# Kernel optimization log

Hardware: AMD Instinct MI355X
Metric: run time of the kernel (lower is better)

Reference implementation:

```python
import jax, jax.numpy as jnp
import numpy as np

T, N, F, S = 512, 64, 256, 1024  # seq_len, batch, behavior features, lstm size


def setup_inputs() -> dict:
    key = jax.random.key(0)
    k1, k2, k3 = jax.random.split(key, 3)
    x = jax.random.normal(k1, (T, N, F), dtype=jnp.float32)
    # stacked gate weights: order [i, f, g, o]
    Wx = jax.random.normal(k2, (4, F, S), dtype=jnp.float32) * 0.02
    Wh = jax.random.normal(k3, (4, S, S), dtype=jnp.float32) * 0.02
    b = jnp.zeros((4, S), dtype=jnp.float32)
    return {"x": x, "Wx": Wx, "Wh": Wh, "b": b}


def reference(x, Wx, Wh, b):
    # x: [T, n, f]; Wx: [4, f, s]; Wh: [4, s, s]; b: [4, s]
    n = x.shape[1]
    s = Wh.shape[-1]
    h0 = jnp.zeros((n, s), dtype=x.dtype)
    c0 = jnp.zeros((n, s), dtype=x.dtype)

    def step(carry, xt):
        h, c = carry
        # fused 4-gate projection: z[k] = xt @ Wx[k] + h @ Wh[k] + b[k]
        z = (jnp.einsum('nf,kfs->kns', xt, Wx)
             + jnp.einsum('ns,kst->knt', h, Wh)
             + b[:, None, :])  # [4, n, s]
        i = jax.nn.sigmoid(z[0])
        f = jax.nn.sigmoid(z[1])
        g = jnp.tanh(z[2])
        o = jax.nn.sigmoid(z[3])
        c = f * c + i * g
        h = o * jnp.tanh(c)
        return (h, c), h

    (_, _), hs = jax.lax.scan(step, (h0, c0), x)
    return hs  # [T, n, s]
```

## Files before the change

### kernel.cpp

```cpp
#include <hip/hip_runtime.h>
#include <hip/hip_bf16.h>

#define T_LEN 512
#define NB 64
#define FB 256
#define SB 1024
#define NWG 256

typedef __attribute__((ext_vector_type(8))) short bf16x8;
typedef __attribute__((ext_vector_type(4))) float f32x4;

#define MFMA(a, b, c) __builtin_amdgcn_mfma_f32_16x16x32_bf16((a), (b), (c), 0, 0, 0)

__device__ __forceinline__ float fast_sigmoid(float z) {
    return 1.f / (1.f + __expf(-z));
}
__device__ __forceinline__ float fast_tanh(float z) {
    return 1.f - 2.f / (1.f + __expf(2.f * z));
}

__device__ __forceinline__ bf16x8 load_frag_dev(const __hip_bfloat16* p) {
    const unsigned long long* q = (const unsigned long long*)p;
    unsigned long long a = __hip_atomic_load(q,     __ATOMIC_RELAXED, __HIP_MEMORY_SCOPE_AGENT);
    unsigned long long b = __hip_atomic_load(q + 1, __ATOMIC_RELAXED, __HIP_MEMORY_SCOPE_AGENT);
    union { unsigned long long u[2]; bf16x8 v; } r;
    r.u[0] = a; r.u[1] = b;
    return r.v;
}

__global__ void xfrag_kernel(const float* __restrict__ x, __hip_bfloat16* __restrict__ xaf) {
    int tid  = blockIdx.x * 256 + threadIdx.x;
    int l    = tid & 63;
    int frag = tid >> 6;
    int kc   = frag & 7;
    int m    = (frag >> 3) & 3;
    int t    = frag >> 5;
    int row  = m * 16 + (l & 15);
    int k0   = kc * 32 + 8 * (l >> 4);
    const float* src = x + ((size_t)(t * NB + row)) * FB + k0;
    __hip_bfloat16* dst = xaf + (size_t)frag * 512 + l * 8;
#pragma unroll
    for (int e = 0; e < 8; ++e) dst[e] = __float2bfloat16(src[e]);
}

__global__ void wfrag_kernel(const float* __restrict__ Wx, const float* __restrict__ Wh,
                             __hip_bfloat16* __restrict__ wbf) {
    int tid  = blockIdx.x * 256 + threadIdx.x;
    int l    = tid & 63;
    int frag = tid >> 6;
    int g    = frag & 3;
    int kcw  = (frag >> 2) % 10;
    int wv   = (frag / 40) & 3;
    int sb   = frag / 160;
    int kc   = (kcw < 2) ? (wv * 2 + kcw) : (8 + wv * 8 + (kcw - 2));
    int s    = sb * 16 + (l & 15);
    int k0   = kc * 32 + 8 * (l >> 4);
    __hip_bfloat16* dst = wbf + (size_t)frag * 512 + l * 8;
#pragma unroll
    for (int e = 0; e < 8; ++e) {
        int k = k0 + e;
        float v = (k < FB) ? Wx[((size_t)g * FB + k) * SB + s]
                           : Wh[((size_t)g * SB + (k - FB)) * SB + s];
        dst[e] = __float2bfloat16(v);
    }
}

__global__ __launch_bounds__(256, 1) void lstm_persist(
    const __hip_bfloat16* __restrict__ xaf,
    const __hip_bfloat16* __restrict__ wbf,
    const float* __restrict__ bias,
    __hip_bfloat16* __restrict__ hfrag,
    float* __restrict__ cbuf,
    float* __restrict__ out,
    unsigned int* __restrict__ flag,
    int t0, int nsteps, int use_sync)
{
    __shared__ float part[4 * 16 * 4 * 17];
    const int tid = threadIdx.x;
    const int wv  = tid >> 6;
    const int l   = tid & 63;
    const int ng  = blockIdx.x >> 6;
    const int sb  = blockIdx.x & 63;
    const int lr  = l & 15;
    const int lg  = l >> 4;

    const int fidx = (ng * 64 + wv * 16 + (l & 15)) * 2;

    const int gn = tid >> 4;
    const int sc = tid & 15;

    bf16x8 wf[40];
    {
        const __hip_bfloat16* wp = wbf + ((size_t)(sb * 4 + wv) * 40) * 512 + l * 8;
#pragma unroll
        for (int i = 0; i < 40; ++i) wf[i] = *reinterpret_cast<const bf16x8*>(wp + (size_t)i * 512);
    }
    float br[4];
#pragma unroll
    for (int g = 0; g < 4; ++g) br[g] = bias[g * SB + sb * 16 + sc];
    float creg = cbuf[(ng * 16 + gn) * SB + sb * 16 + sc];

    const int k8   = 16 * (sb & 1) + sc;
    const int lane = (k8 >> 3) * 16 + gn;
    const size_t hoff = (size_t)((sb >> 1) * 4 + ng) * 512 + lane * 8 + (k8 & 7);

    f32x4 acc[4];
#pragma unroll
    for (int g = 0; g < 4; ++g) acc[g] = (f32x4){0.f, 0.f, 0.f, 0.f};
    {
        const __hip_bfloat16* xs = xaf + (size_t)t0 * 16384;
#pragma unroll
        for (int j = 0; j < 2; ++j) {
            int kc = wv * 2 + j;
            bf16x8 a = *reinterpret_cast<const bf16x8*>(xs + (size_t)(ng * 8 + kc) * 512 + l * 8);
#pragma unroll
            for (int g = 0; g < 4; ++g) acc[g] = MFMA(a, wf[j * 4 + g], acc[g]);
        }
    }

    for (int tt = 0; tt < nsteps; ++tt) {
        const int t = t0 + tt;

        if (use_sync && tt > 0) {
            const unsigned int* f1 = flag + (size_t)(t - 1) * 512;
            for (;;) {
                unsigned a = __hip_atomic_load(&f1[fidx], __ATOMIC_RELAXED, __HIP_MEMORY_SCOPE_AGENT);
                if (__all(a != 0)) break;
            }
            asm volatile("" ::: "memory");
        }

        const __hip_bfloat16* hs = hfrag + (size_t)(t & 3) * 65536;
#pragma unroll
        for (int j = 0; j < 8; ++j) {
            int kch = wv * 8 + j;
            bf16x8 a = load_frag_dev(hs + (size_t)(kch * 4 + ng) * 512 + l * 8);
#pragma unroll
            for (int g = 0; g < 4; ++g) acc[g] = MFMA(a, wf[(2 + j) * 4 + g], acc[g]);
        }

#pragma unroll
        for (int g = 0; g < 4; ++g)
#pragma unroll
            for (int i = 0; i < 4; ++i)
                part[((wv * 16 + lg * 4 + i) * 4 + g) * 17 + lr] = acc[g][i];
        __syncthreads();

        float hv;
        {
            float z[4];
#pragma unroll
            for (int g = 0; g < 4; ++g) {
                float s = 0.f;
#pragma unroll
                for (int w2 = 0; w2 < 4; ++w2)
                    s += part[((w2 * 16 + gn) * 4 + g) * 17 + sc];
                z[g] = s + br[g];
            }
            float ig = fast_sigmoid(z[0]);
            float fg = fast_sigmoid(z[1]);
            float gg = fast_tanh(z[2]);
            float og = fast_sigmoid(z[3]);
            float c  = fg * creg + ig * gg;
            hv       = og * fast_tanh(c);
            creg     = c;
            unsigned short hu = __bfloat16_as_ushort(__float2bfloat16(hv));
            unsigned short* hd = reinterpret_cast<unsigned short*>(
                hfrag + (size_t)((t + 1) & 3) * 65536) + hoff;
            __hip_atomic_store(hd, hu, __ATOMIC_RELAXED, __HIP_MEMORY_SCOPE_AGENT);
        }

        if (use_sync) {
            __syncthreads();
            if (tid == 0)
                __hip_atomic_store(&flag[((size_t)t * 256 + blockIdx.x) * 2], 1u,
                                   __ATOMIC_RELAXED, __HIP_MEMORY_SCOPE_AGENT);
        }

        out[(size_t)t * (NB * SB) + (size_t)(ng * 16 + gn) * SB + sb * 16 + sc] = hv;

        if (tt + 1 < nsteps) {
#pragma unroll
            for (int g = 0; g < 4; ++g) acc[g] = (f32x4){0.f, 0.f, 0.f, 0.f};
            const __hip_bfloat16* xs = xaf + (size_t)(t + 1) * 16384;
#pragma unroll
            for (int j = 0; j < 2; ++j) {
                int kc = wv * 2 + j;
                bf16x8 a = *reinterpret_cast<const bf16x8*>(xs + (size_t)(ng * 8 + kc) * 512 + l * 8);
#pragma unroll
                for (int g = 0; g < 4; ++g) acc[g] = MFMA(a, wf[j * 4 + g], acc[g]);
            }
        }
    }

    cbuf[(ng * 16 + gn) * SB + sb * 16 + sc] = creg;
}

extern "C" void kernel_launch(void* const* d_in, const int* in_sizes, int n_in,
                              void* d_out, int out_size, void* d_ws, size_t ws_size,
                              hipStream_t stream) {
    const float* x  = (const float*)d_in[0];
    const float* Wx = (const float*)d_in[1];
    const float* Wh = (const float*)d_in[2];
    const float* b  = (const float*)d_in[3];
    float* out = (float*)d_out;

    char* ws = (char*)d_ws;
    __hip_bfloat16* xaf   = (__hip_bfloat16*)ws;
    __hip_bfloat16* wbf   = (__hip_bfloat16*)(ws + 16777216);
    __hip_bfloat16* hfrag = (__hip_bfloat16*)(ws + 27262976);
    float*          cbuf  = (float*)(ws + 27787264);
    unsigned int*   flag  = (unsigned int*)(ws + 28049408);

    hipLaunchKernelGGL(xfrag_kernel, dim3(4096), dim3(256), 0, stream, x, xaf);
    hipLaunchKernelGGL(wfrag_kernel, dim3(2560), dim3(256), 0, stream, Wx, Wh, wbf);
    hipMemsetAsync(hfrag, 0, 524288, stream);
    hipMemsetAsync(cbuf, 0, 262144, stream);
    hipMemsetAsync(flag, 0, 1048576, stream);

    const __hip_bfloat16* p_xaf = xaf;
    const __hip_bfloat16* p_wbf = wbf;
    const float* p_bias = b;
    __hip_bfloat16* p_hfrag = hfrag;
    float* p_cbuf = cbuf;
    float* p_out = out;
    unsigned int* p_flag = flag;
    int z0 = 0, ns = T_LEN, us = 1;
    void* args[] = {&p_xaf, &p_wbf, &p_bias, &p_hfrag, &p_cbuf, &p_out, &p_flag, &z0, &ns, &us};
    hipError_t err = hipLaunchCooperativeKernel((void*)lstm_persist, dim3(NWG), dim3(256),
                                                args, 0, stream);
    if (err != hipSuccess) {
        for (int t = 0; t < T_LEN; ++t) {
            hipLaunchKernelGGL(lstm_persist, dim3(NWG), dim3(256), 0, stream,
                               xaf, wbf, b, hfrag, cbuf, out, flag, t, 1, 0);
        }
    }
}
```

Measured before the change: 1.267 ms.

## Halve persistent workgroups and pipeline two independent batch groups per block

Each workgroup now handles two batch groups (A and B) with the same register-resident weights, cutting the grid from 256 to 128 workgroups. The h buffer layout changes so each batch group has its own contiguous ring, and flags are tracked per batch group. Because A and B are independent recurrences, the wait for B's dependencies can overlap with A's gate computation and vice versa. The aim is to hide inter-workgroup synchronisation latency and to halve weight traffic per group. The cost is more serial work per workgroup and twice the accumulator registers.

```diff
diff --git a/kernel.cpp b/kernel.cpp
--- a/kernel.cpp
+++ b/kernel.cpp
@@ -5,7 +5,7 @@
 #define NB 64
 #define FB 256
 #define SB 1024
-#define NWG 256
+#define NWG 128
 
 typedef __attribute__((ext_vector_type(8))) short bf16x8;
 typedef __attribute__((ext_vector_type(4))) float f32x4;
@@ -79,12 +79,13 @@
     const int tid = threadIdx.x;
     const int wv  = tid >> 6;
     const int l   = tid & 63;
-    const int ng  = blockIdx.x >> 6;
+    const int p   = blockIdx.x >> 6;
     const int sb  = blockIdx.x & 63;
     const int lr  = l & 15;
     const int lg  = l >> 4;
-
-    const int fidx = (ng * 64 + wv * 16 + (l & 15)) * 2;
+    const int ngA = 2 * p, ngB = 2 * p + 1;
+
+    const int fbase = (p * 64 + wv * 16 + (l & 15)) * 4;
 
     const int gn = tid >> 4;
     const int sc = tid & 15;
@@ -98,102 +99,157 @@
     float br[4];
 #pragma unroll
     for (int g = 0; g < 4; ++g) br[g] = bias[g * SB + sb * 16 + sc];
-    float creg = cbuf[(ng * 16 + gn) * SB + sb * 16 + sc];
+    float cregA = cbuf[(ngA * 16 + gn) * SB + sb * 16 + sc];
+    float cregB = cbuf[(ngB * 16 + gn) * SB + sb * 16 + sc];
 
     const int k8   = 16 * (sb & 1) + sc;
     const int lane = (k8 >> 3) * 16 + gn;
-    const size_t hoff = (size_t)((sb >> 1) * 4 + ng) * 512 + lane * 8 + (k8 & 7);
-
-    f32x4 acc[4];
-#pragma unroll
-    for (int g = 0; g < 4; ++g) acc[g] = (f32x4){0.f, 0.f, 0.f, 0.f};
+    const int hoff = (sb >> 1) * 512 + lane * 8 + (k8 & 7);
+
+    f32x4 accA[4], accB[4];
+#pragma unroll
+    for (int g = 0; g < 4; ++g) { accA[g] = (f32x4){0,0,0,0}; accB[g] = (f32x4){0,0,0,0}; }
     {
         const __hip_bfloat16* xs = xaf + (size_t)t0 * 16384;
 #pragma unroll
         for (int j = 0; j < 2; ++j) {
             int kc = wv * 2 + j;
-            bf16x8 a = *reinterpret_cast<const bf16x8*>(xs + (size_t)(ng * 8 + kc) * 512 + l * 8);
-#pragma unroll
-            for (int g = 0; g < 4; ++g) acc[g] = MFMA(a, wf[j * 4 + g], acc[g]);
+            bf16x8 aA = *reinterpret_cast<const bf16x8*>(xs + (size_t)(ngA * 8 + kc) * 512 + l * 8);
+            bf16x8 aB = *reinterpret_cast<const bf16x8*>(xs + (size_t)(ngB * 8 + kc) * 512 + l * 8);
+#pragma unroll
+            for (int g = 0; g < 4; ++g) {
+                accA[g] = MFMA(aA, wf[j * 4 + g], accA[g]);
+                accB[g] = MFMA(aB, wf[j * 4 + g], accB[g]);
+            }
         }
     }
 
     for (int tt = 0; tt < nsteps; ++tt) {
         const int t = t0 + tt;
+        const __hip_bfloat16* hsA = hfrag + (size_t)ngA * 65536 + (size_t)(t & 3) * 16384;
+        const __hip_bfloat16* hsB = hfrag + (size_t)ngB * 65536 + (size_t)(t & 3) * 16384;
 
         if (use_sync && tt > 0) {
             const unsigned int* f1 = flag + (size_t)(t - 1) * 512;
             for (;;) {
-                unsigned a = __hip_atomic_load(&f1[fidx], __ATOMIC_RELAXED, __HIP_MEMORY_SCOPE_AGENT);
+                unsigned a = __hip_atomic_load(&f1[fbase], __ATOMIC_RELAXED, __HIP_MEMORY_SCOPE_AGENT);
                 if (__all(a != 0)) break;
             }
             asm volatile("" ::: "memory");
         }
-
-        const __hip_bfloat16* hs = hfrag + (size_t)(t & 3) * 65536;
 #pragma unroll
         for (int j = 0; j < 8; ++j) {
-            int kch = wv * 8 + j;
-            bf16x8 a = load_frag_dev(hs + (size_t)(kch * 4 + ng) * 512 + l * 8);
-#pragma unroll
-            for (int g = 0; g < 4; ++g) acc[g] = MFMA(a, wf[(2 + j) * 4 + g], acc[g]);
-        }
-
+            bf16x8 a = load_frag_dev(hsA + (size_t)(wv * 8 + j) * 512 + l * 8);
+#pragma unroll
+            for (int g = 0; g < 4; ++g) accA[g] = MFMA(a, wf[(2 + j) * 4 + g], accA[g]);
+        }
 #pragma unroll
         for (int g = 0; g < 4; ++g)
 #pragma unroll
             for (int i = 0; i < 4; ++i)
-                part[((wv * 16 + lg * 4 + i) * 4 + g) * 17 + lr] = acc[g][i];
+                part[((wv * 16 + lg * 4 + i) * 4 + g) * 17 + lr] = accA[g][i];
         __syncthreads();
-
-        float hv;
+        float hvA;
         {
             float z[4];
 #pragma unroll
             for (int g = 0; g < 4; ++g) {
                 float s = 0.f;
 #pragma unroll
-                for (int w2 = 0; w2 < 4; ++w2)
-                    s += part[((w2 * 16 + gn) * 4 + g) * 17 + sc];
+                for (int w2 = 0; w2 < 4; ++w2) s += part[((w2 * 16 + gn) * 4 + g) * 17 + sc];
                 z[g] = s + br[g];
             }
             float ig = fast_sigmoid(z[0]);
             float fg = fast_sigmoid(z[1]);
             float gg = fast_tanh(z[2]);
             float og = fast_sigmoid(z[3]);
-            float c  = fg * creg + ig * gg;
-            hv       = og * fast_tanh(c);
-            creg     = c;
-            unsigned short hu = __bfloat16_as_ushort(__float2bfloat16(hv));
+            float c  = fg * cregA + ig * gg;
+            hvA      = og * fast_tanh(c);
+            cregA    = c;
+            unsigned short hu = __bfloat16_as_ushort(__float2bfloat16(hvA));
             unsigned short* hd = reinterpret_cast<unsigned short*>(
-                hfrag + (size_t)((t + 1) & 3) * 65536) + hoff;
+                hfrag + (size_t)ngA * 65536 + (size_t)((t + 1) & 3) * 16384) + hoff;
             __hip_atomic_store(hd, hu, __ATOMIC_RELAXED, __HIP_MEMORY_SCOPE_AGENT);
         }
-
         if (use_sync) {
             __syncthreads();
             if (tid == 0)
-                __hip_atomic_store(&flag[((size_t)t * 256 + blockIdx.x) * 2], 1u,
+                __hip_atomic_store(&flag[((size_t)t * 128 + blockIdx.x) * 4], 1u,
                                    __ATOMIC_RELAXED, __HIP_MEMORY_SCOPE_AGENT);
         }
-
-        out[(size_t)t * (NB * SB) + (size_t)(ng * 16 + gn) * SB + sb * 16 + sc] = hv;
+        out[(size_t)t * (NB * SB) + (size_t)(ngA * 16 + gn) * SB + sb * 16 + sc] = hvA;
+
+        if (use_sync && tt > 0) {
+            const unsigned int* f1 = flag + (size_t)(t - 1) * 512;
+            for (;;) {
+                unsigned a = __hip_atomic_load(&f1[fbase + 1], __ATOMIC_RELAXED, __HIP_MEMORY_SCOPE_AGENT);
+                if (__all(a != 0)) break;
+            }
+            asm volatile("" ::: "memory");
+        }
+#pragma unroll
+        for (int j = 0; j < 8; ++j) {
+            bf16x8 a = load_frag_dev(hsB + (size_t)(wv * 8 + j) * 512 + l * 8);
+#pragma unroll
+            for (int g = 0; g < 4; ++g) accB[g] = MFMA(a, wf[(2 + j) * 4 + g], accB[g]);
+        }
+        if (!use_sync) __syncthreads();
+#pragma unroll
+        for (int g = 0; g < 4; ++g)
+#pragma unroll
+            for (int i = 0; i < 4; ++i)
+                part[((wv * 16 + lg * 4 + i) * 4 + g) * 17 + lr] = accB[g][i];
+        __syncthreads();
+        float hvB;
+        {
+            float z[4];
+#pragma unroll
+            for (int g = 0; g < 4; ++g) {
+                float s = 0.f;
+#pragma unroll
+                for (int w2 = 0; w2 < 4; ++w2) s += part[((w2 * 16 + gn) * 4 + g) * 17 + sc];
+                z[g] = s + br[g];
+            }
+            float ig = fast_sigmoid(z[0]);
+            float fg = fast_sigmoid(z[1]);
+            float gg = fast_tanh(z[2]);
+            float og = fast_sigmoid(z[3]);
+            float c  = fg * cregB + ig * gg;
+            hvB      = og * fast_tanh(c);
+            cregB    = c;
+            unsigned short hu = __bfloat16_as_ushort(__float2bfloat16(hvB));
+            unsigned short* hd = reinterpret_cast<unsigned short*>(
+                hfrag + (size_t)ngB * 65536 + (size_t)((t + 1) & 3) * 16384) + hoff;
+            __hip_atomic_store(hd, hu, __ATOMIC_RELAXED, __HIP_MEMORY_SCOPE_AGENT);
+        }
+        if (use_sync) {
+            __syncthreads();
+            if (tid == 0)
+                __hip_atomic_store(&flag[((size_t)t * 128 + blockIdx.x) * 4 + 1], 1u,
+                                   __ATOMIC_RELAXED, __HIP_MEMORY_SCOPE_AGENT);
+        }
+        out[(size_t)t * (NB * SB) + (size_t)(ngB * 16 + gn) * SB + sb * 16 + sc] = hvB;
 
         if (tt + 1 < nsteps) {
 #pragma unroll
-            for (int g = 0; g < 4; ++g) acc[g] = (f32x4){0.f, 0.f, 0.f, 0.f};
+            for (int g = 0; g < 4; ++g) { accA[g] = (f32x4){0,0,0,0}; accB[g] = (f32x4){0,0,0,0}; }
             const __hip_bfloat16* xs = xaf + (size_t)(t + 1) * 16384;
 #pragma unroll
             for (int j = 0; j < 2; ++j) {
                 int kc = wv * 2 + j;
-                bf16x8 a = *reinterpret_cast<const bf16x8*>(xs + (size_t)(ng * 8 + kc) * 512 + l * 8);
-#pragma unroll
-                for (int g = 0; g < 4; ++g) acc[g] = MFMA(a, wf[j * 4 + g], acc[g]);
-            }
-        }
-    }
-
-    cbuf[(ng * 16 + gn) * SB + sb * 16 + sc] = creg;
+                bf16x8 aA = *reinterpret_cast<const bf16x8*>(xs + (size_t)(ngA * 8 + kc) * 512 + l * 8);
+                bf16x8 aB = *reinterpret_cast<const bf16x8*>(xs + (size_t)(ngB * 8 + kc) * 512 + l * 8);
+#pragma unroll
+                for (int g = 0; g < 4; ++g) {
+                    accA[g] = MFMA(aA, wf[j * 4 + g], accA[g]);
+                    accB[g] = MFMA(aB, wf[j * 4 + g], accB[g]);
+                }
+            }
+        }
+    }
+
+    cbuf[(ngA * 16 + gn) * SB + sb * 16 + sc] = cregA;
+    cbuf[(ngB * 16 + gn) * SB + sb * 16 + sc] = cregB;
 }
 
 extern "C" void kernel_launch(void* const* d_in, const int* in_sizes, int n_in,
```

After: 3.397 ms. 168% more time.

## Replace per-step flag barrier with NaN-sentinel data-driven synchronization

Applied to the files above, without the earlier changes.

The new path gives every timestep its own h buffer, pre-filled with a bf16 NaN sentinel. Consumers spin directly on the h fragments until no sentinel remains, then feed the loaded values straight into MFMA. This removes the flag store, the extra __syncthreads, and the separate flag poll from each step's critical path. In exchange it needs a 64MB workspace plus a large sentinel-init kernel, and it would misbehave if a real h value were the sentinel NaN pattern. The old flag kernel stays as a fallback when the workspace is too small.

```diff
diff --git a/kernel.cpp b/kernel.cpp
--- a/kernel.cpp
+++ b/kernel.cpp
@@ -65,7 +65,147 @@
     }
 }
 
-__global__ __launch_bounds__(256, 1) void lstm_persist(
+__global__ void sentinit_kernel(uint4* __restrict__ p) {
+    p[blockIdx.x * 256 + threadIdx.x] =
+        (uint4){0x7FC07FC0u, 0x7FC07FC0u, 0x7FC07FC0u, 0x7FC07FC0u};
+}
+
+__global__ __launch_bounds__(256, 1) void lstm_ds(
+    const __hip_bfloat16* __restrict__ xaf,
+    const __hip_bfloat16* __restrict__ wbf,
+    const float* __restrict__ bias,
+    __hip_bfloat16* __restrict__ hfrag,
+    float* __restrict__ cbuf,
+    float* __restrict__ out,
+    int t0, int nsteps)
+{
+    __shared__ float part[2][4 * 16 * 4 * 17];
+    const int tid = threadIdx.x;
+    const int wv  = tid >> 6;
+    const int l   = tid & 63;
+    const int ng  = blockIdx.x >> 6;
+    const int sb  = blockIdx.x & 63;
+    const int lr  = l & 15;
+    const int lg  = l >> 4;
+
+    const int gn = tid >> 4;
+    const int sc = tid & 15;
+
+    bf16x8 wf[40];
+    {
+        const __hip_bfloat16* wp = wbf + ((size_t)(sb * 4 + wv) * 40) * 512 + l * 8;
+#pragma unroll
+        for (int i = 0; i < 40; ++i) wf[i] = *reinterpret_cast<const bf16x8*>(wp + (size_t)i * 512);
+    }
+    float br[4];
+#pragma unroll
+    for (int g = 0; g < 4; ++g) br[g] = bias[g * SB + sb * 16 + sc];
+    float creg = cbuf[(ng * 16 + gn) * SB + sb * 16 + sc];
+
+    const int k8   = 16 * (sb & 1) + sc;
+    const int lane = (k8 >> 3) * 16 + gn;
+    const size_t hoff = (size_t)((sb >> 1) * 4 + ng) * 512 + lane * 8 + (k8 & 7);
+
+    f32x4 acc[4];
+#pragma unroll
+    for (int g = 0; g < 4; ++g) acc[g] = (f32x4){0.f, 0.f, 0.f, 0.f};
+    {
+        const __hip_bfloat16* xs = xaf + (size_t)t0 * 16384;
+#pragma unroll
+        for (int j = 0; j < 2; ++j) {
+            int kc = wv * 2 + j;
+            bf16x8 a = *reinterpret_cast<const bf16x8*>(xs + (size_t)(ng * 8 + kc) * 512 + l * 8);
+#pragma unroll
+            for (int g = 0; g < 4; ++g) acc[g] = MFMA(a, wf[j * 4 + g], acc[g]);
+        }
+    }
+
+    for (int tt = 0; tt < nsteps; ++tt) {
+        const int t  = t0 + tt;
+        const int pb = t & 1;
+
+        const __hip_bfloat16* hs = hfrag + (size_t)t * 65536;
+        unsigned long long v[16];
+        for (;;) {
+#pragma unroll
+            for (int j = 0; j < 8; ++j) {
+                const unsigned long long* q = reinterpret_cast<const unsigned long long*>(
+                    hs + (size_t)((wv * 8 + j) * 4 + ng) * 512 + l * 8);
+                v[2 * j]     = __hip_atomic_load(q,     __ATOMIC_RELAXED, __HIP_MEMORY_SCOPE_AGENT);
+                v[2 * j + 1] = __hip_atomic_load(q + 1, __ATOMIC_RELAXED, __HIP_MEMORY_SCOPE_AGENT);
+            }
+            bool ok = true;
+#pragma unroll
+            for (int k = 0; k < 16; ++k) {
+                unsigned lo = (unsigned)v[k], hi = (unsigned)(v[k] >> 32);
+                ok = ok && ((lo & 0xFFFFu) != 0x7FC0u) && ((lo >> 16) != 0x7FC0u)
+                        && ((hi & 0xFFFFu) != 0x7FC0u) && ((hi >> 16) != 0x7FC0u);
+            }
+            if (__all(ok)) break;
+        }
+
+#pragma unroll
+        for (int j = 0; j < 8; ++j) {
+            union { unsigned long long u[2]; bf16x8 a; } ua;
+            ua.u[0] = v[2 * j];
+            ua.u[1] = v[2 * j + 1];
+#pragma unroll
+            for (int g = 0; g < 4; ++g) acc[g] = MFMA(ua.a, wf[(2 + j) * 4 + g], acc[g]);
+        }
+
+#pragma unroll
+        for (int g = 0; g < 4; ++g)
+#pragma unroll
+            for (int i = 0; i < 4; ++i)
+                part[pb][((wv * 16 + lg * 4 + i) * 4 + g) * 17 + lr] = acc[g][i];
+        __syncthreads();
+
+        float hv;
+        {
+            float z[4];
+#pragma unroll
+            for (int g = 0; g < 4; ++g) {
+                float s = 0.f;
+#pragma unroll
+                for (int w2 = 0; w2 < 4; ++w2)
+                    s += part[pb][((w2 * 16 + gn) * 4 + g) * 17 + sc];
+                z[g] = s + br[g];
+            }
+            float ig = fast_sigmoid(z[0]);
+            float fg = fast_sigmoid(z[1]);
+            float gg = fast_tanh(z[2]);
+            float og = fast_sigmoid(z[3]);
+            float c  = fg * creg + ig * gg;
+            hv       = og * fast_tanh(c);
+            creg     = c;
+            if (t + 1 < T_LEN) {
+                unsigned short hu = __bfloat16_as_ushort(__float2bfloat16(hv));
+                unsigned short* hd = reinterpret_cast<unsigned short*>(
+                    hfrag + (size_t)(t + 1) * 65536) + hoff;
+                __hip_atomic_store(hd, hu, __ATOMIC_RELAXED, __HIP_MEMORY_SCOPE_AGENT);
+            }
+        }
+
+        out[(size_t)t * (NB * SB) + (size_t)(ng * 16 + gn) * SB + sb * 16 + sc] = hv;
+
+        if (tt + 1 < nsteps) {
+#pragma unroll
+            for (int g = 0; g < 4; ++g) acc[g] = (f32x4){0.f, 0.f, 0.f, 0.f};
+            const __hip_bfloat16* xs = xaf + (size_t)(t + 1) * 16384;
+#pragma unroll
+            for (int j = 0; j < 2; ++j) {
+                int kc = wv * 2 + j;
+                bf16x8 a = *reinterpret_cast<const bf16x8*>(xs + (size_t)(ng * 8 + kc) * 512 + l * 8);
+#pragma unroll
+                for (int g = 0; g < 4; ++g) acc[g] = MFMA(a, wf[j * 4 + g], acc[g]);
+            }
+        }
+    }
+
+    cbuf[(ng * 16 + gn) * SB + sb * 16 + sc] = creg;
+}
+
+__global__ __launch_bounds__(256, 1) void lstm_fl(
     const __hip_bfloat16* __restrict__ xaf,
     const __hip_bfloat16* __restrict__ wbf,
     const float* __restrict__ bias,
@@ -83,9 +223,7 @@
     const int sb  = blockIdx.x & 63;
     const int lr  = l & 15;
     const int lg  = l >> 4;
-
     const int fidx = (ng * 64 + wv * 16 + (l & 15)) * 2;
-
     const int gn = tid >> 4;
     const int sc = tid & 15;
 
@@ -99,7 +237,6 @@
 #pragma unroll
     for (int g = 0; g < 4; ++g) br[g] = bias[g * SB + sb * 16 + sc];
     float creg = cbuf[(ng * 16 + gn) * SB + sb * 16 + sc];
-
     const int k8   = 16 * (sb & 1) + sc;
     const int lane = (k8 >> 3) * 16 + gn;
     const size_t hoff = (size_t)((sb >> 1) * 4 + ng) * 512 + lane * 8 + (k8 & 7);
@@ -120,7 +257,6 @@
 
     for (int tt = 0; tt < nsteps; ++tt) {
         const int t = t0 + tt;
-
         if (use_sync && tt > 0) {
             const unsigned int* f1 = flag + (size_t)(t - 1) * 512;
             for (;;) {
@@ -129,7 +265,6 @@
             }
             asm volatile("" ::: "memory");
         }
-
         const __hip_bfloat16* hs = hfrag + (size_t)(t & 3) * 65536;
 #pragma unroll
         for (int j = 0; j < 8; ++j) {
@@ -138,14 +273,12 @@
 #pragma unroll
             for (int g = 0; g < 4; ++g) acc[g] = MFMA(a, wf[(2 + j) * 4 + g], acc[g]);
         }
-
 #pragma unroll
         for (int g = 0; g < 4; ++g)
 #pragma unroll
             for (int i = 0; i < 4; ++i)
                 part[((wv * 16 + lg * 4 + i) * 4 + g) * 17 + lr] = acc[g][i];
         __syncthreads();
-
         float hv;
         {
             float z[4];
@@ -153,8 +286,7 @@
             for (int g = 0; g < 4; ++g) {
                 float s = 0.f;
 #pragma unroll
-                for (int w2 = 0; w2 < 4; ++w2)
-                    s += part[((w2 * 16 + gn) * 4 + g) * 17 + sc];
+                for (int w2 = 0; w2 < 4; ++w2) s += part[((w2 * 16 + gn) * 4 + g) * 17 + sc];
                 z[g] = s + br[g];
             }
             float ig = fast_sigmoid(z[0]);
@@ -169,16 +301,13 @@
                 hfrag + (size_t)((t + 1) & 3) * 65536) + hoff;
             __hip_atomic_store(hd, hu, __ATOMIC_RELAXED, __HIP_MEMORY_SCOPE_AGENT);
         }
-
         if (use_sync) {
             __syncthreads();
             if (tid == 0)
                 __hip_atomic_store(&flag[((size_t)t * 256 + blockIdx.x) * 2], 1u,
                                    __ATOMIC_RELAXED, __HIP_MEMORY_SCOPE_AGENT);
         }
-
         out[(size_t)t * (NB * SB) + (size_t)(ng * 16 + gn) * SB + sb * 16 + sc] = hv;
-
         if (tt + 1 < nsteps) {
 #pragma unroll
             for (int g = 0; g < 4; ++g) acc[g] = (f32x4){0.f, 0.f, 0.f, 0.f};
@@ -192,7 +321,6 @@
             }
         }
     }
-
     cbuf[(ng * 16 + gn) * SB + sb * 16 + sc] = creg;
 }
 
@@ -206,33 +334,64 @@
     float* out = (float*)d_out;
 
     char* ws = (char*)d_ws;
-    __hip_bfloat16* xaf   = (__hip_bfloat16*)ws;
-    __hip_bfloat16* wbf   = (__hip_bfloat16*)(ws + 16777216);
-    __hip_bfloat16* hfrag = (__hip_bfloat16*)(ws + 27262976);
-    float*          cbuf  = (float*)(ws + 27787264);
-    unsigned int*   flag  = (unsigned int*)(ws + 28049408);
+    __hip_bfloat16* xaf = (__hip_bfloat16*)ws;
+    __hip_bfloat16* wbf = (__hip_bfloat16*)(ws + 16777216);
 
     hipLaunchKernelGGL(xfrag_kernel, dim3(4096), dim3(256), 0, stream, x, xaf);
     hipLaunchKernelGGL(wfrag_kernel, dim3(2560), dim3(256), 0, stream, Wx, Wh, wbf);
-    hipMemsetAsync(hfrag, 0, 524288, stream);
-    hipMemsetAsync(cbuf, 0, 262144, stream);
-    hipMemsetAsync(flag, 0, 1048576, stream);
-
-    const __hip_bfloat16* p_xaf = xaf;
-    const __hip_bfloat16* p_wbf = wbf;
-    const float* p_bias = b;
-    __hip_bfloat16* p_hfrag = hfrag;
-    float* p_cbuf = cbuf;
-    float* p_out = out;
-    unsigned int* p_flag = flag;
-    int z0 = 0, ns = T_LEN, us = 1;
-    void* args[] = {&p_xaf, &p_wbf, &p_bias, &p_hfrag, &p_cbuf, &p_out, &p_flag, &z0, &ns, &us};
-    hipError_t err = hipLaunchCooperativeKernel((void*)lstm_persist, dim3(NWG), dim3(256),
-                                                args, 0, stream);
-    if (err != hipSuccess) {
-        for (int t = 0; t < T_LEN; ++t) {
-            hipLaunchKernelGGL(lstm_persist, dim3(NWG), dim3(256), 0, stream,
-                               xaf, wbf, b, hfrag, cbuf, out, flag, t, 1, 0);
-        }
-    }
-}
+
+    const size_t NEED = 16777216ULL + 10485760ULL + 67108864ULL + 262144ULL;
+
+    if (ws_size >= NEED) {
+        __hip_bfloat16* hfrag = (__hip_bfloat16*)(ws + 27262976);
+        float*          cbuf  = (float*)(ws + 94371840);
+
+        hipLaunchKernelGGL(sentinit_kernel, dim3(16352), dim3(256), 0, stream,
+                           (uint4*)(hfrag + 65536));
+        hipMemsetAsync(hfrag, 0, 131072, stream);
+        hipMemsetAsync(cbuf, 0, 262144, stream);
+
+        const __hip_bfloat16* p_xaf = xaf;
+        const __hip_bfloat16* p_wbf = wbf;
+        const float* p_bias = b;
+        __hip_bfloat16* p_hfrag = hfrag;
+        float* p_cbuf = cbuf;
+        float* p_out = out;
+        int z0 = 0, ns = T_LEN;
+        void* args[] = {&p_xaf, &p_wbf, &p_bias, &p_hfrag, &p_cbuf, &p_out, &z0, &ns};
+        hipError_t err = hipLaunchCooperativeKernel((void*)lstm_ds, dim3(NWG), dim3(256),
+                                                    args, 0, stream);
+        if (err != hipSuccess) {
+            for (int t = 0; t < T_LEN; ++t) {
+                hipLaunchKernelGGL(lstm_ds, dim3(NWG), dim3(256), 0, stream,
+                                   xaf, wbf, b, hfrag, cbuf, out, t, 1);
+            }
+        }
+    } else {
+        __hip_bfloat16* hfrag = (__hip_bfloat16*)(ws + 27262976);
+        float*          cbuf  = (float*)(ws + 27787264);
+        unsigned int*   flag  = (unsigned int*)(ws + 28049408);
+
+        hipMemsetAsync(hfrag, 0, 524288, stream);
+        hipMemsetAsync(cbuf, 0, 262144, stream);
+        hipMemsetAsync(flag, 0, 1048576, stream);
+
+        const __hip_bfloat16* p_xaf = xaf;
+        const __hip_bfloat16* p_wbf = wbf;
+        const float* p_bias = b;
+        __hip_bfloat16* p_hfrag = hfrag;
+        float* p_cbuf = cbuf;
+        float* p_out = out;
+        unsigned int* p_flag = flag;
+        int z0 = 0, ns = T_LEN, us = 1;
+        void* args[] = {&p_xaf, &p_wbf, &p_bias, &p_hfrag, &p_cbuf, &p_out, &p_flag, &z0, &ns, &us};
+        hipError_t err = hipLaunchCooperativeKernel((void*)lstm_fl, dim3(NWG), dim3(256),
+                                                    args, 0, stream);
+        if (err != hipSuccess) {
+            for (int t = 0; t < T_LEN; ++t) {
+                hipLaunchKernelGGL(lstm_fl, dim3(NWG), dim3(256), 0, stream,
+                                   xaf, wbf, b, hfrag, cbuf, out, flag, t, 1, 0);
+            }
+        }
+    }
+}
```

Measured after the change: 1.418 ms. +12.0%, slower.

## Poll NaN-sentinel hidden-state slots and drop the per-step block barrier

Applied to the files above, without the earlier changes.

The hidden-state buffer becomes one slot per timestep instead of a 4-deep ring, and every slot except the first is pre-filled with a bf16 NaN sentinel by a new init kernel. Each block now re-reads its h fragments until none of them hold the sentinel. Because the data itself is checked, the second __syncthreads before the flag store can go, and the LDS partial-sum buffer is double-buffered so the next step's writes cannot race the current reads. The per-block flag spin stays, so the sentinel check adds polling on top of it. The change also costs a 64MB sentinel fill per launch and assumes a real h value never equals the NaN pattern.

```diff
diff --git a/kernel.cpp b/kernel.cpp
--- a/kernel.cpp
+++ b/kernel.cpp
@@ -65,7 +65,12 @@
     }
 }
 
-__global__ __launch_bounds__(256, 1) void lstm_persist(
+__global__ void sentinit_kernel(uint4* __restrict__ p) {
+    p[blockIdx.x * 256 + threadIdx.x] =
+        (uint4){0x7FC07FC0u, 0x7FC07FC0u, 0x7FC07FC0u, 0x7FC07FC0u};
+}
+
+__global__ __launch_bounds__(256, 1) void lstm_hy(
     const __hip_bfloat16* __restrict__ xaf,
     const __hip_bfloat16* __restrict__ wbf,
     const float* __restrict__ bias,
@@ -75,7 +80,7 @@
     unsigned int* __restrict__ flag,
     int t0, int nsteps, int use_sync)
 {
-    __shared__ float part[4 * 16 * 4 * 17];
+    __shared__ float part[2][4 * 16 * 4 * 17];
     const int tid = threadIdx.x;
     const int wv  = tid >> 6;
     const int l   = tid & 63;
@@ -119,7 +124,8 @@
     }
 
     for (int tt = 0; tt < nsteps; ++tt) {
-        const int t = t0 + tt;
+        const int t  = t0 + tt;
+        const int pb = t & 1;
 
         if (use_sync && tt > 0) {
             const unsigned int* f1 = flag + (size_t)(t - 1) * 512;
@@ -130,20 +136,40 @@
             asm volatile("" ::: "memory");
         }
 
-        const __hip_bfloat16* hs = hfrag + (size_t)(t & 3) * 65536;
+        const __hip_bfloat16* hs = hfrag + (size_t)t * 65536;
+        unsigned long long v[16];
+        for (;;) {
+#pragma unroll
+            for (int j = 0; j < 8; ++j) {
+                const unsigned long long* q = reinterpret_cast<const unsigned long long*>(
+                    hs + (size_t)((wv * 8 + j) * 4 + ng) * 512 + l * 8);
+                v[2 * j]     = __hip_atomic_load(q,     __ATOMIC_RELAXED, __HIP_MEMORY_SCOPE_AGENT);
+                v[2 * j + 1] = __hip_atomic_load(q + 1, __ATOMIC_RELAXED, __HIP_MEMORY_SCOPE_AGENT);
+            }
+            bool ok = true;
+#pragma unroll
+            for (int k = 0; k < 16; ++k) {
+                unsigned lo = (unsigned)v[k], hi = (unsigned)(v[k] >> 32);
+                ok = ok && ((lo & 0xFFFFu) != 0x7FC0u) && ((lo >> 16) != 0x7FC0u)
+                        && ((hi & 0xFFFFu) != 0x7FC0u) && ((hi >> 16) != 0x7FC0u);
+            }
+            if (__all(ok)) break;
+        }
+
 #pragma unroll
         for (int j = 0; j < 8; ++j) {
-            int kch = wv * 8 + j;
-            bf16x8 a = load_frag_dev(hs + (size_t)(kch * 4 + ng) * 512 + l * 8);
-#pragma unroll
-            for (int g = 0; g < 4; ++g) acc[g] = MFMA(a, wf[(2 + j) * 4 + g], acc[g]);
+            union { unsigned long long u[2]; bf16x8 a; } ua;
+            ua.u[0] = v[2 * j];
+            ua.u[1] = v[2 * j + 1];
+#pragma unroll
+            for (int g = 0; g < 4; ++g) acc[g] = MFMA(ua.a, wf[(2 + j) * 4 + g], acc[g]);
         }
 
 #pragma unroll
         for (int g = 0; g < 4; ++g)
 #pragma unroll
             for (int i = 0; i < 4; ++i)
-                part[((wv * 16 + lg * 4 + i) * 4 + g) * 17 + lr] = acc[g][i];
+                part[pb][((wv * 16 + lg * 4 + i) * 4 + g) * 17 + lr] = acc[g][i];
         __syncthreads();
 
         float hv;
@@ -154,7 +180,7 @@
                 float s = 0.f;
 #pragma unroll
                 for (int w2 = 0; w2 < 4; ++w2)
-                    s += part[((w2 * 16 + gn) * 4 + g) * 17 + sc];
+                    s += part[pb][((w2 * 16 + gn) * 4 + g) * 17 + sc];
                 z[g] = s + br[g];
             }
             float ig = fast_sigmoid(z[0]);
@@ -164,15 +190,13 @@
             float c  = fg * creg + ig * gg;
             hv       = og * fast_tanh(c);
             creg     = c;
-            unsigned short hu = __bfloat16_as_ushort(__float2bfloat16(hv));
-            unsigned short* hd = reinterpret_cast<unsigned short*>(
-                hfrag + (size_t)((t + 1) & 3) * 65536) + hoff;
-            __hip_atomic_store(hd, hu, __ATOMIC_RELAXED, __HIP_MEMORY_SCOPE_AGENT);
-        }
-
-        if (use_sync) {
-            __syncthreads();
-            if (tid == 0)
+            if (t + 1 < T_LEN) {
+                unsigned short hu = __bfloat16_as_ushort(__float2bfloat16(hv));
+                unsigned short* hd = reinterpret_cast<unsigned short*>(
+                    hfrag + (size_t)(t + 1) * 65536) + hoff;
+                __hip_atomic_store(hd, hu, __ATOMIC_RELAXED, __HIP_MEMORY_SCOPE_AGENT);
+            }
+            if (use_sync && tid == 0)
                 __hip_atomic_store(&flag[((size_t)t * 256 + blockIdx.x) * 2], 1u,
                                    __ATOMIC_RELAXED, __HIP_MEMORY_SCOPE_AGENT);
         }
@@ -209,12 +233,14 @@
     __hip_bfloat16* xaf   = (__hip_bfloat16*)ws;
     __hip_bfloat16* wbf   = (__hip_bfloat16*)(ws + 16777216);
     __hip_bfloat16* hfrag = (__hip_bfloat16*)(ws + 27262976);
-    float*          cbuf  = (float*)(ws + 27787264);
-    unsigned int*   flag  = (unsigned int*)(ws + 28049408);
+    float*          cbuf  = (float*)(ws + 94371840);
+    unsigned int*   flag  = (unsigned int*)(ws + 94633984);
 
     hipLaunchKernelGGL(xfrag_kernel, dim3(4096), dim3(256), 0, stream, x, xaf);
     hipLaunchKernelGGL(wfrag_kernel, dim3(2560), dim3(256), 0, stream, Wx, Wh, wbf);
-    hipMemsetAsync(hfrag, 0, 524288, stream);
+    hipLaunchKernelGGL(sentinit_kernel, dim3(16352), dim3(256), 0, stream,
+                       (uint4*)(hfrag + 65536));
+    hipMemsetAsync(hfrag, 0, 131072, stream);
     hipMemsetAsync(cbuf, 0, 262144, stream);
     hipMemsetAsync(flag, 0, 1048576, stream);
 
@@ -227,11 +253,11 @@
     unsigned int* p_flag = flag;
     int z0 = 0, ns = T_LEN, us = 1;
     void* args[] = {&p_xaf, &p_wbf, &p_bias, &p_hfrag, &p_cbuf, &p_out, &p_flag, &z0, &ns, &us};
-    hipError_t err = hipLaunchCooperativeKernel((void*)lstm_persist, dim3(NWG), dim3(256),
+    hipError_t err = hipLaunchCooperativeKernel((void*)lstm_hy, dim3(NWG), dim3(256),
                                                 args, 0, stream);
     if (err != hipSuccess) {
         for (int t = 0; t < T_LEN; ++t) {
-            hipLaunchKernelGGL(lstm_persist, dim3(NWG), dim3(256), 0, stream,
+            hipLaunchKernelGGL(lstm_hy, dim3(NWG), dim3(256), 0, stream,
                                xaf, wbf, b, hfrag, cbuf, out, flag, t, 1, 0);
         }
     }
```

Result: slower. 1.403 ms (+10.7%).
